# Kernel tuning notes

Hardware: AMD Instinct MI355X
Metric: run time of the kernel (lower is better)

## Reference

```python
import jax, jax.numpy as jnp
import numpy as np

B, D, L, H = 4, 1024, 2048, 8
HD = D // H


def setup_inputs() -> dict:
    key = jax.random.key(0)
    k1, k2, k3, k4 = jax.random.split(key, 4)
    query = jax.random.normal(k1, (B, D, L), dtype=jnp.float32)
    mask = jax.random.randint(k2, (B, L), 0, 2, dtype=jnp.int32)
    W1 = jax.random.normal(k3, (2 * D, D), dtype=jnp.float32) * (D ** -0.5)
    Wq = jax.random.normal(k4, (D, D), dtype=jnp.float32) * (D ** -0.5)
    return {"query": query, "mask": mask, "W1": W1, "Wq": Wq}


def _split_heads(x):
    # [B, L, C] -> [B, H, L, C//H]
    b, l, c = x.shape
    return x.reshape(b, l, H, c // H).transpose(0, 2, 1, 3)


def reference(query, mask, W1, Wq):
    # 1x1 conv == channel GEMM; produce [B, L, out]
    temp = jnp.einsum('od,bdl->blo', W1, query)   # [B, L, 2D] (K|V)
    q = jnp.einsum('od,bdl->blo', Wq, query)      # [B, L, D]
    k, v = jnp.split(temp, 2, axis=-1)
    q = _split_heads(q) * (HD ** -0.5)            # [B, H, L, HD]
    k = _split_heads(k)
    v = _split_heads(v)
    scores = jnp.einsum('bhqd,bhkd->bhqk', q, k)  # [B, H, L, L]
    m = mask.astype(jnp.float32)[:, None, None, :]
    logits = scores + (-1e30) * (1.0 - m)
    weights = jax.nn.softmax(logits, axis=-1)     # dropout p=0 (eval)
    out = jnp.einsum('bhqk,bhkd->bhqd', weights, v)
    out = out.transpose(0, 2, 1, 3).reshape(B, L, D)  # merge heads
    return out.transpose(0, 2, 1)                 # [B, D, L]
```

## Files before the change

kernel.cpp:

```cpp
#include <hip/hip_runtime.h>
#include <hip/hip_bf16.h>

#define B_  4
#define D_  1024
#define L_  2048
#define H_  8
#define HD_ 128

typedef __attribute__((ext_vector_type(8))) short bf16x8;
typedef __attribute__((ext_vector_type(4))) float f32x4;

static __device__ __forceinline__ ushort f2bf(float f) {
    unsigned u = __float_as_uint(f);
    unsigned r = (u + 0x7fffu + ((u >> 16) & 1u)) >> 16;
    return (ushort)r;
}

static __device__ __forceinline__ void dma16(const ushort* g, ushort* l) {
    __builtin_amdgcn_global_load_lds(
        (const __attribute__((address_space(1))) void*)g,
        (__attribute__((address_space(3))) void*)l, 16, 0, 0);
}

__global__ void k_zero_out(float* __restrict__ out, int n) {
    int i = blockIdx.x * 256 + threadIdx.x;
    if (i < n) out[i] = 0.f;
}

__global__ void k_convert_w(const float* __restrict__ W1, const float* __restrict__ Wq,
                            ushort* __restrict__ Wb) {
    int i = blockIdx.x * 256 + threadIdx.x;
    const int n1 = 2 * D_ * D_ / 4;
    float4 v = (i < n1) ? ((const float4*)W1)[i] : ((const float4*)Wq)[i - n1];
    ushort4 o;
    o.x = f2bf(v.x); o.y = f2bf(v.y); o.z = f2bf(v.z); o.w = f2bf(v.w);
    ((ushort4*)Wb)[i] = o;
}

__global__ void k_transpose(const float* __restrict__ q, ushort* __restrict__ Xt) {
    __shared__ float tile[32][33];
    int b = blockIdx.z, d0 = blockIdx.y * 32, l0 = blockIdx.x * 32;
    int tx = threadIdx.x, ty = threadIdx.y;
    const float* src = q + (size_t)b * D_ * L_;
    for (int i = 0; i < 4; i++)
        tile[ty + 8 * i][tx] = src[(size_t)(d0 + ty + 8 * i) * L_ + l0 + tx];
    __syncthreads();
    ushort* dst = Xt + (size_t)b * L_ * D_;
    for (int i = 0; i < 4; i++)
        dst[(size_t)(l0 + ty + 8 * i) * D_ + d0 + tx] = f2bf(tile[tx][ty + 8 * i]);
}

__global__ void k_scan(const int* __restrict__ mask, int* __restrict__ cidx,
                       int* __restrict__ cnt) {
    int b = blockIdx.x;
    int lane = threadIdx.x;
    const int* mb = mask + b * L_;
    int base = 0;
    for (int c = 0; c < L_; c += 64) {
        int m = mb[c + lane];
        unsigned long long bal = __ballot(m != 0);
        int pre = __popcll(bal & ((1ull << lane) - 1ull));
        if (m) cidx[b * L_ + base + pre] = c + lane;
        base += __popcll(bal);
    }
    for (int j = base + lane; j < L_; j += 64) cidx[b * L_ + j] = 0;
    if (lane == 0) cnt[b] = base;
}

__launch_bounds__(256)
__global__ void k_proj(const ushort* __restrict__ Wb, const ushort* __restrict__ Xt,
                       const int* __restrict__ cidx, const int* __restrict__ cnt,
                       ushort* __restrict__ Qb, ushort* __restrict__ Kb,
                       ushort* __restrict__ Vt) {
    __shared__ alignas(16) ushort As[128 * 64];
    __shared__ alignas(16) ushort Bs[128 * 64];
    const int b  = blockIdx.z;
    const int o0 = blockIdx.y * 128;
    const int l0 = blockIdx.x * 128;
    const int type = o0 >> 10;
    if (type < 2) {
        int tiles = (cnt[b] + 127) >> 7;
        if (blockIdx.x >= tiles) return;
    }
    const int t = threadIdx.x;
    const int wave = t >> 6, lane = t & 63, quad = lane >> 4, li = lane & 15;
    const int wm = wave >> 1, wn = wave & 1;
    const ushort* Xb = Xt + (size_t)b * L_ * D_;

    const int srow = t >> 3;
    const int g = (t & 7) ^ (srow & 7);
    const ushort* aSrc[4];
    const ushort* bSrc[4];
    for (int i = 0; i < 4; i++) {
        int r = i * 32 + srow;
        aSrc[i] = Wb + (size_t)(o0 + r) * D_ + g * 8;
        int l = l0 + r;
        int gl = (type < 2) ? cidx[b * L_ + l] : l;
        bSrc[i] = Xb + (size_t)gl * D_ + g * 8;
    }

    f32x4 acc[4][4] = {};

    for (int k0 = 0; k0 < D_; k0 += 64) {
        for (int i = 0; i < 4; i++)
            dma16(aSrc[i] + k0, &As[(i * 256 + wave * 64) * 8]);
        for (int i = 0; i < 4; i++)
            dma16(bSrc[i] + k0, &Bs[(i * 256 + wave * 64) * 8]);
        __syncthreads();
        for (int ks = 0; ks < 64; ks += 32) {
            const int kc = ks >> 3;
            bf16x8 af[4], bfr[4];
            for (int mf = 0; mf < 4; mf++) {
                int row = wm * 64 + mf * 16 + li;
                af[mf] = *(const bf16x8*)&As[row * 64 + (((kc + quad) ^ (li & 7)) * 8)];
            }
            for (int nf = 0; nf < 4; nf++) {
                int row = wn * 64 + nf * 16 + li;
                bfr[nf] = *(const bf16x8*)&Bs[row * 64 + (((kc + quad) ^ (li & 7)) * 8)];
            }
            for (int mf = 0; mf < 4; mf++)
                for (int nf = 0; nf < 4; nf++)
                    acc[mf][nf] = __builtin_amdgcn_mfma_f32_16x16x32_bf16(af[mf], bfr[nf], acc[mf][nf], 0, 0, 0);
        }
        __syncthreads();
    }

    const float qscale = 0.08838834764831845f;
    for (int mf = 0; mf < 4; mf++) {
        int o = o0 + wm * 64 + mf * 16 + quad * 4;
        int c = o & 1023;
        int h = c >> 7, hd = c & 127;
        for (int nf = 0; nf < 4; nf++) {
            int l = l0 + wn * 64 + nf * 16 + li;
            f32x4 v = acc[mf][nf];
            if (type == 0) {
                ushort4 s4 = { f2bf(v[0]), f2bf(v[1]), f2bf(v[2]), f2bf(v[3]) };
                *(ushort4*)&Kb[(((size_t)(b * H_ + h)) * L_ + l) * HD_ + hd] = s4;
            } else if (type == 1) {
                size_t base = (size_t)(b * H_ + h) * HD_;
                Vt[(base + hd + 0) * L_ + l] = f2bf(v[0]);
                Vt[(base + hd + 1) * L_ + l] = f2bf(v[1]);
                Vt[(base + hd + 2) * L_ + l] = f2bf(v[2]);
                Vt[(base + hd + 3) * L_ + l] = f2bf(v[3]);
            } else {
                ushort4 s4 = { f2bf(v[0] * qscale), f2bf(v[1] * qscale),
                               f2bf(v[2] * qscale), f2bf(v[3] * qscale) };
                *(ushort4*)&Qb[(((size_t)(b * H_ + h)) * L_ + l) * HD_ + hd] = s4;
            }
        }
    }
}

__launch_bounds__(256, 4)
__global__ void k_attn(const ushort* __restrict__ Qb, const ushort* __restrict__ Kb,
                       const ushort* __restrict__ Vt, const int* __restrict__ mask,
                       float* __restrict__ out) {
    __shared__ alignas(16) ushort Ks[2][32][128];
    __shared__ alignas(16) ushort Vs[2][128][32];
    __shared__ alignas(16) ushort Pl[4][16][40];
    const int blk = blockIdx.x;
    const int h = blk & 7, qt = (blk >> 3) & 31, b = blk >> 8;
    const int t = threadIdx.x;
    const int w = t >> 6, lane = t & 63, quad = lane >> 4, li = lane & 15;
    const int q0 = qt * 64 + w * 16;
    const ushort* Qh = Qb + (size_t)(b * H_ + h) * L_ * HD_;
    const ushort* Kh = Kb + (size_t)(b * H_ + h) * L_ * HD_;
    const ushort* Vh = Vt + (size_t)(b * H_ + h) * HD_ * L_;
    const int* mb = mask + b * L_;

    int cm = 0;
    for (int c = lane; c < L_; c += 64) cm += mb[c];
    cm += __shfl_xor(cm, 32, 64);
    cm += __shfl_xor(cm, 16, 64);
    cm += __shfl_xor(cm, 8, 64);
    cm += __shfl_xor(cm, 4, 64);
    cm += __shfl_xor(cm, 2, 64);
    cm += __shfl_xor(cm, 1, 64);
    const int cnt = cm;
    int cnt_pad = (cnt + 31) & ~31;
    if (cnt_pad < 32) cnt_pad = 32;

    const ushort* kgp[2]; const ushort* vgp[2];
    for (int i = 0; i < 2; i++) {
        int seg = w * 2 + i;
        int key = seg * 4 + (lane >> 4);
        int ck  = (lane & 15) ^ (key & 15);
        kgp[i] = Kh + (size_t)key * HD_ + ck * 8;
        int hd  = seg * 16 + (lane >> 2);
        int cv  = (lane & 3) ^ (hd & 3);
        vgp[i] = Vh + (size_t)hd * L_ + cv * 8;
    }

    for (int i = 0; i < 2; i++) dma16(kgp[i], &Ks[0][0][0] + (w * 2 + i) * 512);
    for (int i = 0; i < 2; i++) dma16(vgp[i], &Vs[0][0][0] + (w * 2 + i) * 512);

    bf16x8 qf[4];
    for (int kf = 0; kf < 4; kf++)
        qf[kf] = *(const bf16x8*)&Qh[(size_t)(q0 + li) * HD_ + kf * 32 + quad * 8];

    float mrun = -1e30f, lrun = 0.f;
    f32x4 acc[8] = {};

    int buf = 0;
    for (int n0 = 0; n0 < cnt_pad; n0 += 32, buf ^= 1) {
        __syncthreads();

        if (n0 + 32 < cnt_pad) {
            int nb = buf ^ 1;
            for (int i = 0; i < 2; i++)
                dma16(kgp[i] + (size_t)(n0 + 32) * HD_, &Ks[nb][0][0] + (w * 2 + i) * 512);
            for (int i = 0; i < 2; i++)
                dma16(vgp[i] + (n0 + 32), &Vs[nb][0][0] + (w * 2 + i) * 512);
        }

        f32x4 s[2] = {};
        for (int kf = 0; kf < 4; kf++) {
            bf16x8 kfr[2];
            for (int mt = 0; mt < 2; mt++)
                kfr[mt] = *(const bf16x8*)&Ks[buf][mt * 16 + li][((kf * 4 + quad) ^ li) * 8];
            for (int mt = 0; mt < 2; mt++)
                s[mt] = __builtin_amdgcn_mfma_f32_16x16x32_bf16(kfr[mt], qf[kf], s[mt], 0, 0, 0);
        }

        if (n0 + 32 > cnt) {
            for (int mt = 0; mt < 2; mt++)
                for (int r = 0; r < 4; r++)
                    if (n0 + mt * 16 + quad * 4 + r >= cnt) s[mt][r] = -1e30f;
        }

        float a0 = fmaxf(fmaxf(s[0][0], s[0][1]), fmaxf(s[0][2], s[0][3]));
        float a1 = fmaxf(fmaxf(s[1][0], s[1][1]), fmaxf(s[1][2], s[1][3]));
        float nm = fmaxf(a0, a1);
        nm = fmaxf(nm, __shfl_xor(nm, 16, 64));
        nm = fmaxf(nm, __shfl_xor(nm, 32, 64));
        float mnew = fmaxf(mrun, nm);
        float alpha = __expf(mrun - mnew);
        mrun = mnew;
        float rs = 0.f;
        for (int mt = 0; mt < 2; mt++)
            for (int r = 0; r < 4; r++) {
                float p = __expf(s[mt][r] - mnew);
                s[mt][r] = p;
                rs += p;
            }
        rs += __shfl_xor(rs, 16, 64);
        rs += __shfl_xor(rs, 32, 64);
        lrun = lrun * alpha + rs;

        if (__any(alpha != 1.0f)) {
            int sb = (lane & 48) | (quad * 4);
            float ar0 = __shfl(alpha, sb + 0, 64);
            float ar1 = __shfl(alpha, sb + 1, 64);
            float ar2 = __shfl(alpha, sb + 2, 64);
            float ar3 = __shfl(alpha, sb + 3, 64);
            for (int nf2 = 0; nf2 < 8; nf2++) {
                acc[nf2][0] *= ar0;
                acc[nf2][1] *= ar1;
                acc[nf2][2] *= ar2;
                acc[nf2][3] *= ar3;
            }
        }

        for (int mt = 0; mt < 2; mt++) {
            ushort4 pk = { f2bf(s[mt][0]), f2bf(s[mt][1]),
                           f2bf(s[mt][2]), f2bf(s[mt][3]) };
            *(ushort4*)&Pl[w][li][mt * 16 + quad * 4] = pk;
        }

        bf16x8 pa = *(const bf16x8*)&Pl[w][li][quad * 8];
        for (int nf2 = 0; nf2 < 8; nf2++) {
            bf16x8 vb = *(const bf16x8*)&Vs[buf][nf2 * 16 + li][(quad ^ (li & 3)) * 8];
            acc[nf2] = __builtin_amdgcn_mfma_f32_16x16x32_bf16(pa, vb, acc[nf2], 0, 0, 0);
        }
    }

    float inv = 1.0f / lrun;
    int sb = (lane & 48) | (quad * 4);
    float i0 = __shfl(inv, sb + 0, 64);
    float i1 = __shfl(inv, sb + 1, 64);
    float i2 = __shfl(inv, sb + 2, 64);
    float i3 = __shfl(inv, sb + 3, 64);
    int l = q0 + quad * 4;
    for (int nf2 = 0; nf2 < 8; nf2++) {
        int d = h * HD_ + nf2 * 16 + li;
        float4 o4 = { acc[nf2][0] * i0, acc[nf2][1] * i1,
                      acc[nf2][2] * i2, acc[nf2][3] * i3 };
        *(float4*)&out[((size_t)(b * D_ + d)) * L_ + l] = o4;
    }
}

extern "C" void kernel_launch(void* const* d_in, const int* in_sizes, int n_in,
                              void* d_out, int out_size, void* d_ws, size_t ws_size,
                              hipStream_t stream) {
    const float* query = nullptr;
    const int*   mask  = nullptr;
    const float* W1    = nullptr;
    const float* Wq    = nullptr;
    for (int i = 0; i < n_in; i++) {
        switch (in_sizes[i]) {
            case 8388608: query = (const float*)d_in[i]; break;
            case 8192:    mask  = (const int*)d_in[i];   break;
            case 2097152: W1    = (const float*)d_in[i]; break;
            case 1048576: Wq    = (const float*)d_in[i]; break;
        }
    }
    float* out = (float*)d_out;

    if (ws_size < 50331648u || !query || !mask || !W1 || !Wq) {
        hipLaunchKernelGGL(k_zero_out, dim3((out_size + 255) / 256), dim3(256), 0, stream,
                           out, out_size);
        return;
    }

    ushort* Wb = (ushort*)d_out;
    ushort* Xt = (ushort*)((char*)d_out + 6291456);
    int* cidx  = (int*)((char*)d_out + 23068672);
    int* cnt   = (int*)((char*)d_out + 23101440);
    char* ws = (char*)d_ws;
    ushort* Qb = (ushort*)(ws + 0);
    ushort* Kb = (ushort*)(ws + 16777216);
    ushort* Vt = (ushort*)(ws + 33554432);

    hipLaunchKernelGGL(k_convert_w, dim3(3072), dim3(256), 0, stream, W1, Wq, Wb);
    hipLaunchKernelGGL(k_transpose, dim3(64, 32, 4), dim3(32, 8), 0, stream, query, Xt);
    hipLaunchKernelGGL(k_scan, dim3(4), dim3(64), 0, stream, mask, cidx, cnt);
    hipLaunchKernelGGL(k_proj, dim3(16, 24, 4), dim3(256), 0, stream, Wb, Xt, cidx, cnt, Qb, Kb, Vt);
    hipLaunchKernelGGL(k_attn, dim3(1024), dim3(256), 0, stream, Qb, Kb, Vt, mask, out);
}
```

Measured before the change: 241.8 us.

## Merge prep kernels, fold log2e into Q scale, use exp2 and packed bf16 converts

Merges weight conversion, input transpose and mask scan into one launch that dispatches on block index, cutting two kernel launches. Folds log2(e) into the Q scaling so softmax can use the native exp2 instruction in place of __expf. Replaces the manual bf16 rounding with the hardware packed convert v_cvt_pk_bf16_f32 for K, Q and the P tile. The scan blocks now waste 192 idle threads, and the rounding mode of the hardware convert may differ slightly from the software routine.

```diff
diff --git a/kernel.cpp b/kernel.cpp
--- a/kernel.cpp
+++ b/kernel.cpp
@@ -16,6 +16,20 @@
     return (ushort)r;
 }
 
+static __device__ __forceinline__ unsigned cvt_pk_bf16(float lo, float hi) {
+    unsigned r;
+    asm("v_cvt_pk_bf16_f32 %0, %1, %2" : "=v"(r) : "v"(lo), "v"(hi));
+    return r;
+}
+
+static __device__ __forceinline__ float exp2_fast(float x) {
+#if __has_builtin(__builtin_amdgcn_exp2f)
+    return __builtin_amdgcn_exp2f(x);
+#else
+    return exp2f(x);
+#endif
+}
+
 static __device__ __forceinline__ void dma16(const ushort* g, ushort* l) {
     __builtin_amdgcn_global_load_lds(
         (const __attribute__((address_space(1))) void*)g,
@@ -27,44 +41,47 @@
     if (i < n) out[i] = 0.f;
 }
 
-__global__ void k_convert_w(const float* __restrict__ W1, const float* __restrict__ Wq,
-                            ushort* __restrict__ Wb) {
-    int i = blockIdx.x * 256 + threadIdx.x;
-    const int n1 = 2 * D_ * D_ / 4;
-    float4 v = (i < n1) ? ((const float4*)W1)[i] : ((const float4*)Wq)[i - n1];
-    ushort4 o;
-    o.x = f2bf(v.x); o.y = f2bf(v.y); o.z = f2bf(v.z); o.w = f2bf(v.w);
-    ((ushort4*)Wb)[i] = o;
-}
-
-__global__ void k_transpose(const float* __restrict__ q, ushort* __restrict__ Xt) {
+__global__ void k_prep(const float* __restrict__ q, const float* __restrict__ W1,
+                       const float* __restrict__ Wq, const int* __restrict__ mask,
+                       ushort* __restrict__ Wb, ushort* __restrict__ Xt,
+                       int* __restrict__ cidx, int* __restrict__ cnt) {
     __shared__ float tile[32][33];
-    int b = blockIdx.z, d0 = blockIdx.y * 32, l0 = blockIdx.x * 32;
-    int tx = threadIdx.x, ty = threadIdx.y;
-    const float* src = q + (size_t)b * D_ * L_;
-    for (int i = 0; i < 4; i++)
-        tile[ty + 8 * i][tx] = src[(size_t)(d0 + ty + 8 * i) * L_ + l0 + tx];
-    __syncthreads();
-    ushort* dst = Xt + (size_t)b * L_ * D_;
-    for (int i = 0; i < 4; i++)
-        dst[(size_t)(l0 + ty + 8 * i) * D_ + d0 + tx] = f2bf(tile[tx][ty + 8 * i]);
-}
-
-__global__ void k_scan(const int* __restrict__ mask, int* __restrict__ cidx,
-                       int* __restrict__ cnt) {
-    int b = blockIdx.x;
-    int lane = threadIdx.x;
-    const int* mb = mask + b * L_;
-    int base = 0;
-    for (int c = 0; c < L_; c += 64) {
-        int m = mb[c + lane];
-        unsigned long long bal = __ballot(m != 0);
-        int pre = __popcll(bal & ((1ull << lane) - 1ull));
-        if (m) cidx[b * L_ + base + pre] = c + lane;
-        base += __popcll(bal);
-    }
-    for (int j = base + lane; j < L_; j += 64) cidx[b * L_ + j] = 0;
-    if (lane == 0) cnt[b] = base;
+    const int bid = blockIdx.x, t = threadIdx.x;
+    if (bid < 8192) {
+        int bx = bid & 63, by = (bid >> 6) & 31, bz = bid >> 11;
+        int tx = t & 31, ty = t >> 5;
+        int d0 = by * 32, l0 = bx * 32;
+        const float* src = q + (size_t)bz * D_ * L_;
+        for (int i = 0; i < 4; i++)
+            tile[ty + 8 * i][tx] = src[(size_t)(d0 + ty + 8 * i) * L_ + l0 + tx];
+        __syncthreads();
+        ushort* dst = Xt + (size_t)bz * L_ * D_;
+        for (int i = 0; i < 4; i++)
+            dst[(size_t)(l0 + ty + 8 * i) * D_ + d0 + tx] = f2bf(tile[tx][ty + 8 * i]);
+    } else if (bid < 8192 + 3072) {
+        int i = (bid - 8192) * 256 + t;
+        const int n1 = 2 * D_ * D_ / 4;
+        float4 v = (i < n1) ? ((const float4*)W1)[i] : ((const float4*)Wq)[i - n1];
+        ushort4 o;
+        o.x = f2bf(v.x); o.y = f2bf(v.y); o.z = f2bf(v.z); o.w = f2bf(v.w);
+        ((ushort4*)Wb)[i] = o;
+    } else {
+        int b = bid - (8192 + 3072);
+        if (t < 64) {
+            int lane = t;
+            const int* mb = mask + b * L_;
+            int base = 0;
+            for (int c = 0; c < L_; c += 64) {
+                int m = mb[c + lane];
+                unsigned long long bal = __ballot(m != 0);
+                int pre = __popcll(bal & ((1ull << lane) - 1ull));
+                if (m) cidx[b * L_ + base + pre] = c + lane;
+                base += __popcll(bal);
+            }
+            for (int j = base + lane; j < L_; j += 64) cidx[b * L_ + j] = 0;
+            if (lane == 0) cnt[b] = base;
+        }
+    }
 }
 
 __launch_bounds__(256)
@@ -125,7 +142,7 @@
         __syncthreads();
     }
 
-    const float qscale = 0.08838834764831845f;
+    const float qscale = 0.1275174495450826f;
     for (int mf = 0; mf < 4; mf++) {
         int o = o0 + wm * 64 + mf * 16 + quad * 4;
         int c = o & 1023;
@@ -134,8 +151,10 @@
             int l = l0 + wn * 64 + nf * 16 + li;
             f32x4 v = acc[mf][nf];
             if (type == 0) {
-                ushort4 s4 = { f2bf(v[0]), f2bf(v[1]), f2bf(v[2]), f2bf(v[3]) };
-                *(ushort4*)&Kb[(((size_t)(b * H_ + h)) * L_ + l) * HD_ + hd] = s4;
+                uint2 kk;
+                kk.x = cvt_pk_bf16(v[0], v[1]);
+                kk.y = cvt_pk_bf16(v[2], v[3]);
+                *(uint2*)&Kb[(((size_t)(b * H_ + h)) * L_ + l) * HD_ + hd] = kk;
             } else if (type == 1) {
                 size_t base = (size_t)(b * H_ + h) * HD_;
                 Vt[(base + hd + 0) * L_ + l] = f2bf(v[0]);
@@ -143,9 +162,10 @@
                 Vt[(base + hd + 2) * L_ + l] = f2bf(v[2]);
                 Vt[(base + hd + 3) * L_ + l] = f2bf(v[3]);
             } else {
-                ushort4 s4 = { f2bf(v[0] * qscale), f2bf(v[1] * qscale),
-                               f2bf(v[2] * qscale), f2bf(v[3] * qscale) };
-                *(ushort4*)&Qb[(((size_t)(b * H_ + h)) * L_ + l) * HD_ + hd] = s4;
+                uint2 qq;
+                qq.x = cvt_pk_bf16(v[0] * qscale, v[1] * qscale);
+                qq.y = cvt_pk_bf16(v[2] * qscale, v[3] * qscale);
+                *(uint2*)&Qb[(((size_t)(b * H_ + h)) * L_ + l) * HD_ + hd] = qq;
             }
         }
     }
@@ -234,12 +254,12 @@
         nm = fmaxf(nm, __shfl_xor(nm, 16, 64));
         nm = fmaxf(nm, __shfl_xor(nm, 32, 64));
         float mnew = fmaxf(mrun, nm);
-        float alpha = __expf(mrun - mnew);
+        float alpha = exp2_fast(mrun - mnew);
         mrun = mnew;
         float rs = 0.f;
         for (int mt = 0; mt < 2; mt++)
             for (int r = 0; r < 4; r++) {
-                float p = __expf(s[mt][r] - mnew);
+                float p = exp2_fast(s[mt][r] - mnew);
                 s[mt][r] = p;
                 rs += p;
             }
@@ -262,9 +282,10 @@
         }
 
         for (int mt = 0; mt < 2; mt++) {
-            ushort4 pk = { f2bf(s[mt][0]), f2bf(s[mt][1]),
-                           f2bf(s[mt][2]), f2bf(s[mt][3]) };
-            *(ushort4*)&Pl[w][li][mt * 16 + quad * 4] = pk;
+            uint2 pk;
+            pk.x = cvt_pk_bf16(s[mt][0], s[mt][1]);
+            pk.y = cvt_pk_bf16(s[mt][2], s[mt][3]);
+            *(uint2*)&Pl[w][li][mt * 16 + quad * 4] = pk;
         }
 
         bf16x8 pa = *(const bf16x8*)&Pl[w][li][quad * 8];
@@ -321,9 +342,8 @@
     ushort* Kb = (ushort*)(ws + 16777216);
     ushort* Vt = (ushort*)(ws + 33554432);
 
-    hipLaunchKernelGGL(k_convert_w, dim3(3072), dim3(256), 0, stream, W1, Wq, Wb);
-    hipLaunchKernelGGL(k_transpose, dim3(64, 32, 4), dim3(32, 8), 0, stream, query, Xt);
-    hipLaunchKernelGGL(k_scan, dim3(4), dim3(64), 0, stream, mask, cidx, cnt);
+    hipLaunchKernelGGL(k_prep, dim3(8192 + 3072 + 4), dim3(256), 0, stream,
+                       query, W1, Wq, mask, Wb, Xt, cidx, cnt);
     hipLaunchKernelGGL(k_proj, dim3(16, 24, 4), dim3(256), 0, stream, Wb, Xt, cidx, cnt, Qb, Kb, Vt);
     hipLaunchKernelGGL(k_attn, dim3(1024), dim3(256), 0, stream, Qb, Kb, Vt, mask, out);
 }
```

Result: faster. 232.0 us (-4.0%).
